# Kernel tuning notes

Measured on AMD Instinct MI355X. Metric: run time of the kernel, lower is better.

The kernel has to match this reference:

```python
import jax, jax.numpy as jnp
import numpy as np

B, S, D = 2, 2048, 1024
H = 16
HD = D // H  # 64
FORESIGHT = -1e9  # masked_fill value for non-causal positions


def setup_inputs() -> dict:
    key = jax.random.key(0)
    ks = jax.random.split(key, 8)
    s = 0.02
    return {
        "x": jax.random.normal(ks[0], (B, S, D), dtype=jnp.float32),
        "Wq": jax.random.normal(ks[1], (D, H * HD), dtype=jnp.float32) * s,
        "bq": jax.random.normal(ks[2], (H * HD,), dtype=jnp.float32) * s,
        "Wk": jax.random.normal(ks[3], (D, H * HD), dtype=jnp.float32) * s,
        "Wv": jax.random.normal(ks[4], (D, H * HD), dtype=jnp.float32) * s,
        "Wo": jax.random.normal(ks[5], (H * HD, D), dtype=jnp.float32) * s,
        "bo": jax.random.normal(ks[6], (D,), dtype=jnp.float32) * s,
    }


def reference(x, Wq, bq, Wk, Wv, Wo, bo):
    b, s, _ = x.shape
    # projections -> [B, H, S, HD]
    q = (x @ Wq + bq).reshape(b, s, H, HD).transpose(0, 2, 1, 3)
    k = (x @ Wk).reshape(b, s, H, HD).transpose(0, 2, 1, 3)
    v = (x @ Wv).reshape(b, s, H, HD).transpose(0, 2, 1, 3)
    # scores [B, H, S, S]
    scores = jnp.einsum("bhqd,bhkd->bhqk", q, k) / jnp.sqrt(jnp.float32(HD))
    # ALiBi bias: slope_h * j (key position), broadcast over queries
    slopes = 2.0 ** (-8.0 * jnp.arange(1, H + 1, dtype=jnp.float32) / H)
    positions = jnp.arange(s, dtype=jnp.float32)
    scores = scores - slopes[None, :, None, None] * positions[None, None, None, :]
    # causal mask: fill strictly-upper triangle with foresight
    causal = jnp.tril(jnp.ones((s, s), dtype=bool))
    scores = jnp.where(causal[None, None, :, :], scores, FORESIGHT)
    attn = jax.nn.softmax(scores, axis=-1)
    out = jnp.einsum("bhqk,bhkd->bhqd", attn, v)
    out = out.transpose(0, 2, 1, 3).reshape(b, s, H * HD)
    return out @ Wo + bo
```

## Files before the change

### kernel.cpp

```cpp
#include <hip/hip_runtime.h>
#include <stdint.h>

#define DDIM 1024
#define HH 16
#define HDIM 64
#define SS 2048

typedef short bf16x8 __attribute__((ext_vector_type(8)));
typedef float f32x4 __attribute__((ext_vector_type(4)));
typedef unsigned short u16;

__device__ __forceinline__ unsigned f2bf(float f) {
  unsigned u = __builtin_bit_cast(unsigned, f);
  u = u + 0x7FFFu + ((u >> 16) & 1u);
  return u >> 16;
}

__device__ __forceinline__ unsigned cvt_pk_bf16(float a, float b) {
  unsigned r;
  asm("v_cvt_pk_bf16_f32 %0, %1, %2" : "=v"(r) : "v"(a), "v"(b));
  return r;
}

__device__ __forceinline__ void gload16(const void* g, void* l) {
  __builtin_amdgcn_global_load_lds(
      (const __attribute__((address_space(1))) unsigned int*)g,
      (__attribute__((address_space(3))) unsigned int*)l, 16, 0, 0);
}

__global__ void k_convert_x(const float* __restrict__ x, u16* __restrict__ xb) {
  int i = (blockIdx.x * 256 + threadIdx.x) * 4;
  float4 v = *(const float4*)(x + i);
  ushort4 o;
  o.x = (u16)f2bf(v.x); o.y = (u16)f2bf(v.y); o.z = (u16)f2bf(v.z); o.w = (u16)f2bf(v.w);
  *(ushort4*)(xb + i) = o;
}

__global__ void k_transpose_w(const float* __restrict__ w0, const float* __restrict__ w1,
                              const float* __restrict__ w2, const float* __restrict__ w3,
                              u16* __restrict__ wt) {
  __shared__ float t[64][65];
  int z = blockIdx.z;
  const float* src = (z == 0) ? w0 : (z == 1) ? w1 : (z == 2) ? w2 : w3;
  u16* dst = wt + (size_t)z * DDIM * DDIM;
  int k0 = blockIdx.x * 64, n0 = blockIdx.y * 64;
  int tid = threadIdx.x;
  int c4 = tid & 15, rr = tid >> 4;
  for (int rep = 0; rep < 4; rep++) {
    int r = rr + rep * 16;
    float4 v = *(const float4*)(src + (size_t)(k0 + r) * DDIM + n0 + c4 * 4);
    t[r][c4 * 4 + 0] = v.x; t[r][c4 * 4 + 1] = v.y;
    t[r][c4 * 4 + 2] = v.z; t[r][c4 * 4 + 3] = v.w;
  }
  __syncthreads();
  for (int rep = 0; rep < 4; rep++) {
    int n = rr + rep * 16;
    ushort4 o;
    o.x = (u16)f2bf(t[c4 * 4 + 0][n]); o.y = (u16)f2bf(t[c4 * 4 + 1][n]);
    o.z = (u16)f2bf(t[c4 * 4 + 2][n]); o.w = (u16)f2bf(t[c4 * 4 + 3][n]);
    *(ushort4*)(dst + (size_t)(n0 + n) * DDIM + k0 + c4 * 4) = o;
  }
}

template <int MODE>
__global__ __launch_bounds__(256, 2) void k_gemm(const u16* __restrict__ A,
                                                 const u16* __restrict__ BT,
                                                 const float* __restrict__ bias,
                                                 void* __restrict__ O0,
                                                 void* __restrict__ O1,
                                                 void* __restrict__ O2) {
  __shared__ __align__(16) u16 lA[128 * 64];
  __shared__ __align__(16) u16 lB[128 * 64];
  const int tid = threadIdx.x;
  const int l = tid & 63, w = tid >> 6;
  const int wm = w >> 1, wn = w & 1;
  const int m0 = blockIdx.x * 128, n0 = blockIdx.y * 128;
  const int lr = l >> 4, lc = l & 15;

  const int srow = l >> 3;
  const int scol = ((l & 7) ^ srow) * 8;

  f32x4 acc[4][4];
  for (int mi = 0; mi < 4; mi++)
    for (int ni = 0; ni < 4; ni++)
      acc[mi][ni] = f32x4{0.f, 0.f, 0.f, 0.f};

  for (int kk = 0; kk < 16; kk++) {
    const int k0 = kk * 64;
    for (int i = 0; i < 4; i++) {
      int c = w * 4 + i;
      gload16(A + (size_t)(m0 + c * 8 + srow) * DDIM + k0 + scol, (char*)lA + c * 1024);
      gload16(BT + (size_t)(n0 + c * 8 + srow) * DDIM + k0 + scol, (char*)lB + c * 1024);
    }
    __syncthreads();
    for (int ks = 0; ks < 2; ks++) {
      bf16x8 af[4], bfr[4];
      for (int mi = 0; mi < 4; mi++) {
        int row = wm * 64 + mi * 16 + lc;
        int slot = (ks * 4 + lr) ^ (row & 7);
        af[mi] = *(const bf16x8*)((const char*)lA + row * 128 + slot * 16);
      }
      for (int ni = 0; ni < 4; ni++) {
        int row = wn * 64 + ni * 16 + lc;
        int slot = (ks * 4 + lr) ^ (row & 7);
        bfr[ni] = *(const bf16x8*)((const char*)lB + row * 128 + slot * 16);
      }
      for (int mi = 0; mi < 4; mi++)
        for (int ni = 0; ni < 4; ni++)
          acc[mi][ni] = __builtin_amdgcn_mfma_f32_16x16x32_bf16(af[mi], bfr[ni], acc[mi][ni], 0, 0, 0);
    }
    __syncthreads();
  }

  if (MODE == 0) {
    const int which = blockIdx.y >> 3;
    if (which == 0) {
      u16* C = (u16*)O0;
      const float c1 = 0.18033688011112043f;
      for (int mi = 0; mi < 4; mi++)
        for (int ni = 0; ni < 4; ni++) {
          int nl = (n0 + wn * 64 + ni * 16 + lc) & 1023;
          float badd = bias[nl];
          for (int r = 0; r < 4; r++) {
            int m = m0 + wm * 64 + mi * 16 + lr * 4 + r;
            C[(size_t)m * DDIM + nl] = (u16)f2bf((acc[mi][ni][r] + badd) * c1);
          }
        }
    } else if (which == 1) {
      u16* C = (u16*)O1;
      for (int mi = 0; mi < 4; mi++)
        for (int ni = 0; ni < 4; ni++) {
          int nl = (n0 + wn * 64 + ni * 16 + lc) & 1023;
          for (int r = 0; r < 4; r++) {
            int m = m0 + wm * 64 + mi * 16 + lr * 4 + r;
            C[(size_t)m * DDIM + nl] = (u16)f2bf(acc[mi][ni][r]);
          }
        }
    } else {
      u16* C = (u16*)O2;
      for (int mi = 0; mi < 4; mi++)
        for (int ni = 0; ni < 4; ni++) {
          int nl = (n0 + wn * 64 + ni * 16 + lc) & 1023;
          int h = nl >> 6, hd = nl & 63;
          int m = m0 + wm * 64 + mi * 16 + lr * 4;
          int b = m >> 11, s = m & 2047;
          unsigned d0 = f2bf(acc[mi][ni][0]) | (f2bf(acc[mi][ni][1]) << 16);
          unsigned d1 = f2bf(acc[mi][ni][2]) | (f2bf(acc[mi][ni][3]) << 16);
          u16* p = C + ((size_t)((b * HH + h) * HDIM + hd)) * SS + s;
          *(unsigned*)(p) = d0;
          *(unsigned*)(p + 2) = d1;
        }
    }
  } else {
    float* C = (float*)O0;
    for (int mi = 0; mi < 4; mi++)
      for (int ni = 0; ni < 4; ni++) {
        int n = n0 + wn * 64 + ni * 16 + lc;
        float badd = bias[n];
        for (int r = 0; r < 4; r++) {
          int m = m0 + wm * 64 + mi * 16 + lr * 4 + r;
          C[(size_t)m * DDIM + n] = acc[mi][ni][r] + badd;
        }
      }
  }
}

__device__ __forceinline__ void attn_tile(int kt, bool masked, int kfhi,
                                          const char* lKc, const char* lVc, char* lPw,
                                          const bf16x8 qf[2], f32x4 of[4],
                                          float& mrun, float& lrun_lane,
                                          float slope2, int lr, int lc, int q_glob) {
  f32x4 sf[4];
#pragma unroll
  for (int kf = 0; kf < 4; kf++) sf[kf] = f32x4{0.f, 0.f, 0.f, 0.f};
  __builtin_amdgcn_s_setprio(1);
#pragma unroll
  for (int ks = 0; ks < 2; ks++)
#pragma unroll
    for (int kf = 0; kf < 4; kf++) {
      if (kf >= kfhi) continue;
      int key = kf * 16 + lc;
      int slot = (ks * 4 + lr) ^ (lc & 7);
      bf16x8 a = *(const bf16x8*)(lKc + key * 128 + slot * 16);
      sf[kf] = __builtin_amdgcn_mfma_f32_16x16x32_bf16(a, qf[ks], sf[kf], 0, 0, 0);
    }
  __builtin_amdgcn_s_setprio(0);

  const float base = -slope2 * (float)(kt * 64 + lr * 4);
  float tmax = -3.0e38f;
#pragma unroll
  for (int kf = 0; kf < 4; kf++) {
    if (kf >= kfhi) continue;
#pragma unroll
    for (int r = 0; r < 4; r++) {
      float sv = sf[kf][r] + (base - slope2 * (float)(kf * 16 + r));
      if (masked) {
        int key = kt * 64 + kf * 16 + lr * 4 + r;
        if (key > q_glob) sv = -3.0e38f;
      }
      sf[kf][r] = sv;
      tmax = fmaxf(tmax, sv);
    }
  }

  if (__any(tmax > mrun)) {
    float tcol = fmaxf(tmax, __shfl_xor(tmax, 16));
    tcol = fmaxf(tcol, __shfl_xor(tcol, 32));
    if (tcol > mrun) {
      float corr = exp2f(mrun - tcol);
      lrun_lane *= corr;
#pragma unroll
      for (int mf = 0; mf < 4; mf++) {
        of[mf][0] *= corr; of[mf][1] *= corr; of[mf][2] *= corr; of[mf][3] *= corr;
      }
      mrun = tcol;
    }
  }

  const int kfUp = (kfhi + 1) & ~1;
  f32x4 ps = f32x4{0.f, 0.f, 0.f, 0.f};
#pragma unroll
  for (int kf = 0; kf < 4; kf++) {
    if (kf >= kfUp) continue;
    uint2 uu;
    if (kf < kfhi) {
      float p0 = exp2f(sf[kf][0] - mrun);
      float p1 = exp2f(sf[kf][1] - mrun);
      float p2 = exp2f(sf[kf][2] - mrun);
      float p3 = exp2f(sf[kf][3] - mrun);
      ps[0] += p0; ps[1] += p1; ps[2] += p2; ps[3] += p3;
      uu.x = cvt_pk_bf16(p0, p1);
      uu.y = cvt_pk_bf16(p2, p3);
    } else {
      uu.x = 0u; uu.y = 0u;
    }
    int slot = ((kf * 2 + (lr >> 1)) ^ (lc & 7));
    *(uint2*)(lPw + lc * 128 + slot * 16 + (lr & 1) * 8) = uu;
  }
  lrun_lane += (ps[0] + ps[1]) + (ps[2] + ps[3]);

  const int kshi = kfUp >> 1;
  __builtin_amdgcn_s_setprio(1);
#pragma unroll
  for (int ks = 0; ks < 2; ks++) {
    if (ks >= kshi) continue;
    int slotp = (ks * 4 + lr) ^ (lc & 7);
    bf16x8 pb = *(const bf16x8*)(lPw + lc * 128 + slotp * 16);
#pragma unroll
    for (int mf = 0; mf < 4; mf++) {
      int hd = mf * 16 + lc;
      int slotv = (ks * 4 + lr) ^ (lc & 7);
      bf16x8 va = *(const bf16x8*)(lVc + hd * 128 + slotv * 16);
      of[mf] = __builtin_amdgcn_mfma_f32_16x16x32_bf16(va, pb, of[mf], 0, 0, 0);
    }
  }
  __builtin_amdgcn_s_setprio(0);
}

__global__ __launch_bounds__(256, 4) void k_attn(const u16* __restrict__ Q,
                                                 const u16* __restrict__ Kg,
                                                 const u16* __restrict__ Vt,
                                                 u16* __restrict__ AO) {
  __shared__ __align__(16) u16 lK[2][64 * 64];
  __shared__ __align__(16) u16 lV[2][64 * 64];
  __shared__ __align__(16) u16 lP[4][16 * 64];

  const int tid = threadIdx.x;
  const int l = tid & 63, w = tid >> 6;
  const int lr = l >> 4, lc = l & 15;
  const int id = blockIdx.x;
  const int bh = id & 31;
  const int s5 = (id >> 5) & 1;
  const int gg = id >> 6;
  const int qt = s5 ? (31 - gg) : gg;
  const int b = bh >> 4, h = bh & 15;

  const float slope2 = exp2f(-0.5f * (float)(h + 1)) * 1.4426950408889634f;
  const int q_glob = qt * 64 + w * 16 + lc;

  bf16x8 qf[2];
#pragma unroll
  for (int ks = 0; ks < 2; ks++)
    qf[ks] = *(const bf16x8*)(Q + (size_t)(b * SS + q_glob) * DDIM + h * HDIM + ks * 32 + lr * 8);

  f32x4 of[4];
#pragma unroll
  for (int mf = 0; mf < 4; mf++) of[mf] = f32x4{0.f, 0.f, 0.f, 0.f};
  float mrun = -3.0e38f, lrun_lane = 0.f;

  const int srow = l >> 3;
  const int scol = ((l & 7) ^ srow) * 8;
  const int nkt = qt + 1;
  char* lPw = (char*)lP[w];

  auto stage = [&](int kt, int bb) {
#pragma unroll
    for (int i = 0; i < 2; i++) {
      int c = i * 4 + w;
      gload16(Kg + (size_t)(b * SS + kt * 64 + c * 8 + srow) * DDIM + h * HDIM + scol,
              (char*)lK[bb] + c * 1024);
      gload16(Vt + ((size_t)bh * HDIM + c * 8 + srow) * SS + kt * 64 + scol,
              (char*)lV[bb] + c * 1024);
    }
  };

  stage(0, 0);
  stage(nkt > 1 ? 1 : 0, 1);

  for (int t = 0; t < nkt; t++) {
    asm volatile("s_waitcnt vmcnt(4)" ::: "memory");
    __builtin_amdgcn_s_barrier();
    asm volatile("" ::: "memory");
    const bool last = (t == nkt - 1);
    attn_tile(t, last, last ? (w + 1) : 4,
              (const char*)lK[t & 1], (const char*)lV[t & 1], lPw,
              qf, of, mrun, lrun_lane, slope2, lr, lc, q_glob);
    __builtin_amdgcn_s_barrier();
    asm volatile("" ::: "memory");
    int kts = t + 2;
    if (kts > nkt - 1) kts = nkt - 1;
    stage(kts, t & 1);
  }

  float lrun = lrun_lane;
  lrun += __shfl_xor(lrun, 16);
  lrun += __shfl_xor(lrun, 32);
  float inv = 1.f / lrun;
  u16* obase = AO + (size_t)(b * SS + q_glob) * DDIM + h * HDIM;
#pragma unroll
  for (int mf = 0; mf < 4; mf++) {
    uint2 uu;
    uu.x = cvt_pk_bf16(of[mf][0] * inv, of[mf][1] * inv);
    uu.y = cvt_pk_bf16(of[mf][2] * inv, of[mf][3] * inv);
    *(uint2*)(obase + mf * 16 + lr * 4) = uu;
  }
}

extern "C" void kernel_launch(void* const* d_in, const int* in_sizes, int n_in,
                              void* d_out, int out_size, void* d_ws, size_t ws_size,
                              hipStream_t stream) {
  const float* x  = (const float*)d_in[0];
  const float* Wq = (const float*)d_in[1];
  const float* bq = (const float*)d_in[2];
  const float* Wk = (const float*)d_in[3];
  const float* Wv = (const float*)d_in[4];
  const float* Wo = (const float*)d_in[5];
  const float* bo = (const float*)d_in[6];
  float* out = (float*)d_out;

  u16* ws = (u16*)d_ws;
  const size_t MEG = 1024 * 1024;
  u16* xb = ws;
  u16* WT = ws + 4 * MEG;
  u16* Qb = ws + 8 * MEG;
  u16* Kb = ws + 12 * MEG;
  u16* Vt = ws + 16 * MEG;
  u16* AO = ws + 20 * MEG;

  k_convert_x<<<dim3(4096), dim3(256), 0, stream>>>(x, xb);
  k_transpose_w<<<dim3(16, 16, 4), dim3(256), 0, stream>>>(Wq, Wk, Wv, Wo, WT);
  k_gemm<0><<<dim3(32, 24), dim3(256), 0, stream>>>(xb, WT, bq, (void*)Qb, (void*)Kb, (void*)Vt);
  k_attn<<<dim3(1024), dim3(256), 0, stream>>>(Qb, Kb, Vt, AO);
  k_gemm<1><<<dim3(32, 8), dim3(256), 0, stream>>>(AO, WT + 3 * MEG, bo, (void*)out, nullptr, nullptr);
}
```

Measured before the change: 121.7 us.

## Pair complementary causal query tiles per block to share K/V staging

Each attention block now handles two query tiles, gg and 31-gg, for the same head. The K/V tiles staged into LDS are reused by both query streams, which balances causal work per block and halves K/V global loads. The grid is halved to 512 blocks and the occupancy hint drops from 4 to 3, in exchange for more registers (two sets of accumulators) and a larger P buffer. This gives fewer resident waves and fewer blocks to spread across CUs.

```diff
diff --git a/kernel.cpp b/kernel.cpp
--- a/kernel.cpp
+++ b/kernel.cpp
@@ -165,15 +165,14 @@
   }
 }
 
-__device__ __forceinline__ void attn_tile(int kt, bool masked, int kfhi,
-                                          const char* lKc, const char* lVc, char* lPw,
-                                          const bf16x8 qf[2], f32x4 of[4],
-                                          float& mrun, float& lrun_lane,
-                                          float slope2, int lr, int lc, int q_glob) {
+__device__ __forceinline__ void attn_stream(int kt, bool masked, int kfhi,
+                                            const char* lKc, const char* lVc, char* lPw,
+                                            const bf16x8 qf[2], f32x4 of[4],
+                                            float& mrun, float& lrun_lane,
+                                            float slope2, int lr, int lc, int q_glob) {
   f32x4 sf[4];
 #pragma unroll
   for (int kf = 0; kf < 4; kf++) sf[kf] = f32x4{0.f, 0.f, 0.f, 0.f};
-  __builtin_amdgcn_s_setprio(1);
 #pragma unroll
   for (int ks = 0; ks < 2; ks++)
 #pragma unroll
@@ -184,7 +183,6 @@
       bf16x8 a = *(const bf16x8*)(lKc + key * 128 + slot * 16);
       sf[kf] = __builtin_amdgcn_mfma_f32_16x16x32_bf16(a, qf[ks], sf[kf], 0, 0, 0);
     }
-  __builtin_amdgcn_s_setprio(0);
 
   const float base = -slope2 * (float)(kt * 64 + lr * 4);
   float tmax = -3.0e38f;
@@ -240,7 +238,6 @@
   lrun_lane += (ps[0] + ps[1]) + (ps[2] + ps[3]);
 
   const int kshi = kfUp >> 1;
-  __builtin_amdgcn_s_setprio(1);
 #pragma unroll
   for (int ks = 0; ks < 2; ks++) {
     if (ks >= kshi) continue;
@@ -254,44 +251,50 @@
       of[mf] = __builtin_amdgcn_mfma_f32_16x16x32_bf16(va, pb, of[mf], 0, 0, 0);
     }
   }
-  __builtin_amdgcn_s_setprio(0);
-}
-
-__global__ __launch_bounds__(256, 4) void k_attn(const u16* __restrict__ Q,
+}
+
+__global__ __launch_bounds__(256, 3) void k_attn(const u16* __restrict__ Q,
                                                  const u16* __restrict__ Kg,
                                                  const u16* __restrict__ Vt,
                                                  u16* __restrict__ AO) {
   __shared__ __align__(16) u16 lK[2][64 * 64];
   __shared__ __align__(16) u16 lV[2][64 * 64];
-  __shared__ __align__(16) u16 lP[4][16 * 64];
+  __shared__ __align__(16) u16 lP[4][2][16 * 64];
 
   const int tid = threadIdx.x;
   const int l = tid & 63, w = tid >> 6;
   const int lr = l >> 4, lc = l & 15;
   const int id = blockIdx.x;
   const int bh = id & 31;
-  const int s5 = (id >> 5) & 1;
-  const int gg = id >> 6;
-  const int qt = s5 ? (31 - gg) : gg;
+  const int gg = id >> 5;
+  const int qtA = gg, qtB = 31 - gg;
   const int b = bh >> 4, h = bh & 15;
 
   const float slope2 = exp2f(-0.5f * (float)(h + 1)) * 1.4426950408889634f;
-  const int q_glob = qt * 64 + w * 16 + lc;
-
-  bf16x8 qf[2];
-#pragma unroll
-  for (int ks = 0; ks < 2; ks++)
-    qf[ks] = *(const bf16x8*)(Q + (size_t)(b * SS + q_glob) * DDIM + h * HDIM + ks * 32 + lr * 8);
-
-  f32x4 of[4];
-#pragma unroll
-  for (int mf = 0; mf < 4; mf++) of[mf] = f32x4{0.f, 0.f, 0.f, 0.f};
-  float mrun = -3.0e38f, lrun_lane = 0.f;
+  const int q_globA = qtA * 64 + w * 16 + lc;
+  const int q_globB = qtB * 64 + w * 16 + lc;
+
+  bf16x8 qfA[2], qfB[2];
+#pragma unroll
+  for (int ks = 0; ks < 2; ks++) {
+    qfA[ks] = *(const bf16x8*)(Q + (size_t)(b * SS + q_globA) * DDIM + h * HDIM + ks * 32 + lr * 8);
+    qfB[ks] = *(const bf16x8*)(Q + (size_t)(b * SS + q_globB) * DDIM + h * HDIM + ks * 32 + lr * 8);
+  }
+
+  f32x4 ofA[4], ofB[4];
+#pragma unroll
+  for (int mf = 0; mf < 4; mf++) {
+    ofA[mf] = f32x4{0.f, 0.f, 0.f, 0.f};
+    ofB[mf] = f32x4{0.f, 0.f, 0.f, 0.f};
+  }
+  float mrunA = -3.0e38f, lrA = 0.f;
+  float mrunB = -3.0e38f, lrB = 0.f;
 
   const int srow = l >> 3;
   const int scol = ((l & 7) ^ srow) * 8;
-  const int nkt = qt + 1;
-  char* lPw = (char*)lP[w];
+  const int nkt = qtB + 1;
+  char* lPA = (char*)lP[w][0];
+  char* lPB = (char*)lP[w][1];
 
   auto stage = [&](int kt, int bb) {
 #pragma unroll
@@ -305,16 +308,26 @@
   };
 
   stage(0, 0);
-  stage(nkt > 1 ? 1 : 0, 1);
+  stage(1, 1);
 
   for (int t = 0; t < nkt; t++) {
     asm volatile("s_waitcnt vmcnt(4)" ::: "memory");
     __builtin_amdgcn_s_barrier();
     asm volatile("" ::: "memory");
-    const bool last = (t == nkt - 1);
-    attn_tile(t, last, last ? (w + 1) : 4,
-              (const char*)lK[t & 1], (const char*)lV[t & 1], lPw,
-              qf, of, mrun, lrun_lane, slope2, lr, lc, q_glob);
+    const char* Kc = (const char*)lK[t & 1];
+    const char* Vc = (const char*)lV[t & 1];
+    __builtin_amdgcn_s_setprio(1);
+    {
+      const bool lastB = (t == qtB);
+      attn_stream(t, lastB, lastB ? (w + 1) : 4, Kc, Vc, lPB,
+                  qfB, ofB, mrunB, lrB, slope2, lr, lc, q_globB);
+      if (t <= qtA) {
+        const bool lastA = (t == qtA);
+        attn_stream(t, lastA, lastA ? (w + 1) : 4, Kc, Vc, lPA,
+                    qfA, ofA, mrunA, lrA, slope2, lr, lc, q_globA);
+      }
+    }
+    __builtin_amdgcn_s_setprio(0);
     __builtin_amdgcn_s_barrier();
     asm volatile("" ::: "memory");
     int kts = t + 2;
@@ -322,17 +335,33 @@
     stage(kts, t & 1);
   }
 
-  float lrun = lrun_lane;
-  lrun += __shfl_xor(lrun, 16);
-  lrun += __shfl_xor(lrun, 32);
-  float inv = 1.f / lrun;
-  u16* obase = AO + (size_t)(b * SS + q_glob) * DDIM + h * HDIM;
-#pragma unroll
-  for (int mf = 0; mf < 4; mf++) {
-    uint2 uu;
-    uu.x = cvt_pk_bf16(of[mf][0] * inv, of[mf][1] * inv);
-    uu.y = cvt_pk_bf16(of[mf][2] * inv, of[mf][3] * inv);
-    *(uint2*)(obase + mf * 16 + lr * 4) = uu;
+  {
+    float lrun = lrA;
+    lrun += __shfl_xor(lrun, 16);
+    lrun += __shfl_xor(lrun, 32);
+    float inv = 1.f / lrun;
+    u16* obase = AO + (size_t)(b * SS + q_globA) * DDIM + h * HDIM;
+#pragma unroll
+    for (int mf = 0; mf < 4; mf++) {
+      uint2 uu;
+      uu.x = cvt_pk_bf16(ofA[mf][0] * inv, ofA[mf][1] * inv);
+      uu.y = cvt_pk_bf16(ofA[mf][2] * inv, ofA[mf][3] * inv);
+      *(uint2*)(obase + mf * 16 + lr * 4) = uu;
+    }
+  }
+  {
+    float lrun = lrB;
+    lrun += __shfl_xor(lrun, 16);
+    lrun += __shfl_xor(lrun, 32);
+    float inv = 1.f / lrun;
+    u16* obase = AO + (size_t)(b * SS + q_globB) * DDIM + h * HDIM;
+#pragma unroll
+    for (int mf = 0; mf < 4; mf++) {
+      uint2 uu;
+      uu.x = cvt_pk_bf16(ofB[mf][0] * inv, ofB[mf][1] * inv);
+      uu.y = cvt_pk_bf16(ofB[mf][2] * inv, ofB[mf][3] * inv);
+      *(uint2*)(obase + mf * 16 + lr * 4) = uu;
+    }
   }
 }
 
@@ -360,6 +389,6 @@
   k_convert_x<<<dim3(4096), dim3(256), 0, stream>>>(x, xb);
   k_transpose_w<<<dim3(16, 16, 4), dim3(256), 0, stream>>>(Wq, Wk, Wv, Wo, WT);
   k_gemm<0><<<dim3(32, 24), dim3(256), 0, stream>>>(xb, WT, bq, (void*)Qb, (void*)Kb, (void*)Vt);
-  k_attn<<<dim3(1024), dim3(256), 0, stream>>>(Qb, Kb, Vt, AO);
+  k_attn<<<dim3(512), dim3(256), 0, stream>>>(Qb, Kb, Vt, AO);
   k_gemm<1><<<dim3(32, 8), dim3(256), 0, stream>>>(AO, WT + 3 * MEG, bo, (void*)out, nullptr, nullptr);
 }
```

Result: slower. 126.0 us (+3.6%).

## Rewrite attention with 32x32 MFMA, register-resident P via permlane swap

Applied to the files above, without the earlier changes.

The attention kernel now gives each wave 32 queries and uses 32x32x16 bf16 MFMAs for both QK^T and PV. The P matrix is repacked in registers with v_permlane32_swap instead of a round trip through LDS. Each block now covers 128 queries and its four waves share one K/V stream, so the grid halves to 512 blocks and launch bounds drop to 2 blocks per CU. The goal is fewer LDS accesses and MFMA instructions per tile and more K/V reuse. The costs are more registers per wave, lower occupancy, and waves in a block sitting idle on different numbers of tiles.

```diff
diff --git a/kernel.cpp b/kernel.cpp
--- a/kernel.cpp
+++ b/kernel.cpp
@@ -8,6 +8,7 @@
 
 typedef short bf16x8 __attribute__((ext_vector_type(8)));
 typedef float f32x4 __attribute__((ext_vector_type(4)));
+typedef float f32x16 __attribute__((ext_vector_type(16)));
 typedef unsigned short u16;
 
 __device__ __forceinline__ unsigned f2bf(float f) {
@@ -22,10 +23,21 @@
   return r;
 }
 
+__device__ __forceinline__ void pswap(unsigned& a, unsigned& b) {
+  asm volatile("v_permlane32_swap_b32 %0, %1" : "+v"(a), "+v"(b));
+}
+
 __device__ __forceinline__ void gload16(const void* g, void* l) {
   __builtin_amdgcn_global_load_lds(
       (const __attribute__((address_space(1))) unsigned int*)g,
       (__attribute__((address_space(3))) unsigned int*)l, 16, 0, 0);
+}
+
+__device__ __forceinline__ f32x16 zero16() {
+  f32x16 z;
+#pragma unroll
+  for (int r = 0; r < 16; r++) z[r] = 0.f;
+  return z;
 }
 
 __global__ void k_convert_x(const float* __restrict__ x, u16* __restrict__ xb) {
@@ -165,133 +177,43 @@
   }
 }
 
-__device__ __forceinline__ void attn_tile(int kt, bool masked, int kfhi,
-                                          const char* lKc, const char* lVc, char* lPw,
-                                          const bf16x8 qf[2], f32x4 of[4],
-                                          float& mrun, float& lrun_lane,
-                                          float slope2, int lr, int lc, int q_glob) {
-  f32x4 sf[4];
-#pragma unroll
-  for (int kf = 0; kf < 4; kf++) sf[kf] = f32x4{0.f, 0.f, 0.f, 0.f};
-  __builtin_amdgcn_s_setprio(1);
-#pragma unroll
-  for (int ks = 0; ks < 2; ks++)
-#pragma unroll
-    for (int kf = 0; kf < 4; kf++) {
-      if (kf >= kfhi) continue;
-      int key = kf * 16 + lc;
-      int slot = (ks * 4 + lr) ^ (lc & 7);
-      bf16x8 a = *(const bf16x8*)(lKc + key * 128 + slot * 16);
-      sf[kf] = __builtin_amdgcn_mfma_f32_16x16x32_bf16(a, qf[ks], sf[kf], 0, 0, 0);
-    }
-  __builtin_amdgcn_s_setprio(0);
-
-  const float base = -slope2 * (float)(kt * 64 + lr * 4);
-  float tmax = -3.0e38f;
-#pragma unroll
-  for (int kf = 0; kf < 4; kf++) {
-    if (kf >= kfhi) continue;
-#pragma unroll
-    for (int r = 0; r < 4; r++) {
-      float sv = sf[kf][r] + (base - slope2 * (float)(kf * 16 + r));
-      if (masked) {
-        int key = kt * 64 + kf * 16 + lr * 4 + r;
-        if (key > q_glob) sv = -3.0e38f;
-      }
-      sf[kf][r] = sv;
-      tmax = fmaxf(tmax, sv);
-    }
-  }
-
-  if (__any(tmax > mrun)) {
-    float tcol = fmaxf(tmax, __shfl_xor(tmax, 16));
-    tcol = fmaxf(tcol, __shfl_xor(tcol, 32));
-    if (tcol > mrun) {
-      float corr = exp2f(mrun - tcol);
-      lrun_lane *= corr;
-#pragma unroll
-      for (int mf = 0; mf < 4; mf++) {
-        of[mf][0] *= corr; of[mf][1] *= corr; of[mf][2] *= corr; of[mf][3] *= corr;
-      }
-      mrun = tcol;
-    }
-  }
-
-  const int kfUp = (kfhi + 1) & ~1;
-  f32x4 ps = f32x4{0.f, 0.f, 0.f, 0.f};
-#pragma unroll
-  for (int kf = 0; kf < 4; kf++) {
-    if (kf >= kfUp) continue;
-    uint2 uu;
-    if (kf < kfhi) {
-      float p0 = exp2f(sf[kf][0] - mrun);
-      float p1 = exp2f(sf[kf][1] - mrun);
-      float p2 = exp2f(sf[kf][2] - mrun);
-      float p3 = exp2f(sf[kf][3] - mrun);
-      ps[0] += p0; ps[1] += p1; ps[2] += p2; ps[3] += p3;
-      uu.x = cvt_pk_bf16(p0, p1);
-      uu.y = cvt_pk_bf16(p2, p3);
-    } else {
-      uu.x = 0u; uu.y = 0u;
-    }
-    int slot = ((kf * 2 + (lr >> 1)) ^ (lc & 7));
-    *(uint2*)(lPw + lc * 128 + slot * 16 + (lr & 1) * 8) = uu;
-  }
-  lrun_lane += (ps[0] + ps[1]) + (ps[2] + ps[3]);
-
-  const int kshi = kfUp >> 1;
-  __builtin_amdgcn_s_setprio(1);
-#pragma unroll
-  for (int ks = 0; ks < 2; ks++) {
-    if (ks >= kshi) continue;
-    int slotp = (ks * 4 + lr) ^ (lc & 7);
-    bf16x8 pb = *(const bf16x8*)(lPw + lc * 128 + slotp * 16);
-#pragma unroll
-    for (int mf = 0; mf < 4; mf++) {
-      int hd = mf * 16 + lc;
-      int slotv = (ks * 4 + lr) ^ (lc & 7);
-      bf16x8 va = *(const bf16x8*)(lVc + hd * 128 + slotv * 16);
-      of[mf] = __builtin_amdgcn_mfma_f32_16x16x32_bf16(va, pb, of[mf], 0, 0, 0);
-    }
-  }
-  __builtin_amdgcn_s_setprio(0);
-}
-
-__global__ __launch_bounds__(256, 4) void k_attn(const u16* __restrict__ Q,
+__global__ __launch_bounds__(256, 2) void k_attn(const u16* __restrict__ Q,
                                                  const u16* __restrict__ Kg,
                                                  const u16* __restrict__ Vt,
                                                  u16* __restrict__ AO) {
   __shared__ __align__(16) u16 lK[2][64 * 64];
   __shared__ __align__(16) u16 lV[2][64 * 64];
-  __shared__ __align__(16) u16 lP[4][16 * 64];
 
   const int tid = threadIdx.x;
   const int l = tid & 63, w = tid >> 6;
-  const int lr = l >> 4, lc = l & 15;
+  const int lq = l & 31, hi = l >> 5;
   const int id = blockIdx.x;
   const int bh = id & 31;
-  const int s5 = (id >> 5) & 1;
-  const int gg = id >> 6;
-  const int qt = s5 ? (31 - gg) : gg;
+  const int gslot = id >> 5;
+  const int g = (gslot < 8) ? gslot : 23 - gslot;
   const int b = bh >> 4, h = bh & 15;
+  const int sw = g * 4 + w;
+  const int qglob = sw * 32 + lq;
+  const int nktw = (sw >> 1) + 1;
+  const int nkt = 2 * g + 2;
 
   const float slope2 = exp2f(-0.5f * (float)(h + 1)) * 1.4426950408889634f;
-  const int q_glob = qt * 64 + w * 16 + lc;
-
-  bf16x8 qf[2];
-#pragma unroll
-  for (int ks = 0; ks < 2; ks++)
-    qf[ks] = *(const bf16x8*)(Q + (size_t)(b * SS + q_glob) * DDIM + h * HDIM + ks * 32 + lr * 8);
-
-  f32x4 of[4];
-#pragma unroll
-  for (int mf = 0; mf < 4; mf++) of[mf] = f32x4{0.f, 0.f, 0.f, 0.f};
-  float mrun = -3.0e38f, lrun_lane = 0.f;
+  const float sh4 = slope2 * (float)(4 * hi);
+
+  f32x16 scr;
+#pragma unroll
+  for (int r = 0; r < 16; r++) scr[r] = slope2 * (float)((r & 3) + 8 * (r >> 2));
+
+  bf16x8 qf[4];
+#pragma unroll
+  for (int sd = 0; sd < 4; sd++)
+    qf[sd] = *(const bf16x8*)(Q + (size_t)(b * SS + qglob) * DDIM + h * HDIM + sd * 16 + hi * 8);
+
+  f32x16 o0 = zero16(), o1 = zero16();
+  float mrun = -3.0e38f, lrl = 0.f;
 
   const int srow = l >> 3;
   const int scol = ((l & 7) ^ srow) * 8;
-  const int nkt = qt + 1;
-  char* lPw = (char*)lP[w];
 
   auto stage = [&](int kt, int bb) {
 #pragma unroll
@@ -305,16 +227,123 @@
   };
 
   stage(0, 0);
-  stage(nkt > 1 ? 1 : 0, 1);
+  stage(1, 1);
 
   for (int t = 0; t < nkt; t++) {
     asm volatile("s_waitcnt vmcnt(4)" ::: "memory");
     __builtin_amdgcn_s_barrier();
     asm volatile("" ::: "memory");
-    const bool last = (t == nkt - 1);
-    attn_tile(t, last, last ? (w + 1) : 4,
-              (const char*)lK[t & 1], (const char*)lV[t & 1], lPw,
-              qf, of, mrun, lrun_lane, slope2, lr, lc, q_glob);
+    if (t < nktw) {
+      const char* Kc = (const char*)lK[t & 1];
+      const char* Vc = (const char*)lV[t & 1];
+      const bool lastp = (t == nktw - 1);
+      const bool doT1 = !lastp || (sw & 1);
+      const bool mT0 = lastp && !(sw & 1);
+      const bool mT1 = lastp && (sw & 1);
+
+      f32x16 s0 = zero16(), s1 = zero16();
+      __builtin_amdgcn_s_setprio(1);
+#pragma unroll
+      for (int sd = 0; sd < 4; sd++) {
+        int row = lq;
+        int slot = (2 * sd + hi) ^ (row & 7);
+        bf16x8 a = *(const bf16x8*)(Kc + row * 128 + slot * 16);
+        s0 = __builtin_amdgcn_mfma_f32_32x32x16_bf16(a, qf[sd], s0, 0, 0, 0);
+      }
+      if (doT1) {
+#pragma unroll
+        for (int sd = 0; sd < 4; sd++) {
+          int row = 32 + lq;
+          int slot = (2 * sd + hi) ^ (row & 7);
+          bf16x8 a = *(const bf16x8*)(Kc + row * 128 + slot * 16);
+          s1 = __builtin_amdgcn_mfma_f32_32x32x16_bf16(a, qf[sd], s1, 0, 0, 0);
+        }
+      }
+      __builtin_amdgcn_s_setprio(0);
+
+      const float bt0 = -slope2 * (float)(t * 64) - sh4;
+      const float bt1 = bt0 - slope2 * 32.f;
+      float tmax = -3.0e38f;
+#pragma unroll
+      for (int r = 0; r < 16; r++) {
+        float sv = (s0[r] + bt0) - scr[r];
+        if (mT0) {
+          int key = t * 64 + (r & 3) + 8 * (r >> 2) + 4 * hi;
+          if (key > qglob) sv = -3.0e38f;
+        }
+        s0[r] = sv;
+        tmax = fmaxf(tmax, sv);
+      }
+      if (doT1) {
+#pragma unroll
+        for (int r = 0; r < 16; r++) {
+          float sv = (s1[r] + bt1) - scr[r];
+          if (mT1) {
+            int key = t * 64 + 32 + (r & 3) + 8 * (r >> 2) + 4 * hi;
+            if (key > qglob) sv = -3.0e38f;
+          }
+          s1[r] = sv;
+          tmax = fmaxf(tmax, sv);
+        }
+      }
+      float tcol = fmaxf(tmax, __shfl_xor(tmax, 32));
+      if (__any(tcol > mrun)) {
+        float mnew = fmaxf(mrun, tcol);
+        float corr = exp2f(mrun - mnew);
+        lrl *= corr;
+#pragma unroll
+        for (int r = 0; r < 16; r++) { o0[r] *= corr; o1[r] *= corr; }
+        mrun = mnew;
+      }
+
+      f32x4 ps = f32x4{0.f, 0.f, 0.f, 0.f};
+#pragma unroll
+      for (int r = 0; r < 16; r++) {
+        float p = exp2f(s0[r] - mrun);
+        s0[r] = p;
+        ps[r & 3] += p;
+      }
+      if (doT1) {
+#pragma unroll
+        for (int r = 0; r < 16; r++) {
+          float p = exp2f(s1[r] - mrun);
+          s1[r] = p;
+          ps[r & 3] += p;
+        }
+      }
+      lrl += (ps[0] + ps[1]) + (ps[2] + ps[3]);
+
+      __builtin_amdgcn_s_setprio(1);
+      auto pvstep = [&](const f32x16& cs, int s) {
+        const int b8 = (s & 1) * 8;
+        unsigned x1 = cvt_pk_bf16(cs[b8 + 0], cs[b8 + 1]);
+        unsigned y1 = cvt_pk_bf16(cs[b8 + 4], cs[b8 + 5]);
+        pswap(x1, y1);
+        unsigned x2 = cvt_pk_bf16(cs[b8 + 2], cs[b8 + 3]);
+        unsigned y2 = cvt_pk_bf16(cs[b8 + 6], cs[b8 + 7]);
+        pswap(x2, y2);
+        uint4 pw; pw.x = x1; pw.y = x2; pw.z = y1; pw.w = y2;
+        bf16x8 pb = __builtin_bit_cast(bf16x8, pw);
+        int slotb = 2 * s + hi;
+        {
+          int row = lq;
+          bf16x8 va = *(const bf16x8*)(Vc + row * 128 + ((slotb ^ (row & 7)) << 4));
+          o0 = __builtin_amdgcn_mfma_f32_32x32x16_bf16(va, pb, o0, 0, 0, 0);
+        }
+        {
+          int row = 32 + lq;
+          bf16x8 va = *(const bf16x8*)(Vc + row * 128 + ((slotb ^ (row & 7)) << 4));
+          o1 = __builtin_amdgcn_mfma_f32_32x32x16_bf16(va, pb, o1, 0, 0, 0);
+        }
+      };
+      pvstep(s0, 0);
+      pvstep(s0, 1);
+      if (doT1) {
+        pvstep(s1, 2);
+        pvstep(s1, 3);
+      }
+      __builtin_amdgcn_s_setprio(0);
+    }
     __builtin_amdgcn_s_barrier();
     asm volatile("" ::: "memory");
     int kts = t + 2;
@@ -322,17 +351,18 @@
     stage(kts, t & 1);
   }
 
-  float lrun = lrun_lane;
-  lrun += __shfl_xor(lrun, 16);
-  lrun += __shfl_xor(lrun, 32);
-  float inv = 1.f / lrun;
-  u16* obase = AO + (size_t)(b * SS + q_glob) * DDIM + h * HDIM;
-#pragma unroll
-  for (int mf = 0; mf < 4; mf++) {
+  float lcol = lrl + __shfl_xor(lrl, 32);
+  float inv = 1.f / lcol;
+  u16* obase = AO + (size_t)(b * SS + qglob) * DDIM + h * HDIM;
+#pragma unroll
+  for (int rg = 0; rg < 4; rg++) {
     uint2 uu;
-    uu.x = cvt_pk_bf16(of[mf][0] * inv, of[mf][1] * inv);
-    uu.y = cvt_pk_bf16(of[mf][2] * inv, of[mf][3] * inv);
-    *(uint2*)(obase + mf * 16 + lr * 4) = uu;
+    uu.x = cvt_pk_bf16(o0[4 * rg + 0] * inv, o0[4 * rg + 1] * inv);
+    uu.y = cvt_pk_bf16(o0[4 * rg + 2] * inv, o0[4 * rg + 3] * inv);
+    *(uint2*)(obase + rg * 8 + 4 * hi) = uu;
+    uu.x = cvt_pk_bf16(o1[4 * rg + 0] * inv, o1[4 * rg + 1] * inv);
+    uu.y = cvt_pk_bf16(o1[4 * rg + 2] * inv, o1[4 * rg + 3] * inv);
+    *(uint2*)(obase + 32 + rg * 8 + 4 * hi) = uu;
   }
 }
 
@@ -360,6 +390,6 @@
   k_convert_x<<<dim3(4096), dim3(256), 0, stream>>>(x, xb);
   k_transpose_w<<<dim3(16, 16, 4), dim3(256), 0, stream>>>(Wq, Wk, Wv, Wo, WT);
   k_gemm<0><<<dim3(32, 24), dim3(256), 0, stream>>>(xb, WT, bq, (void*)Qb, (void*)Kb, (void*)Vt);
-  k_attn<<<dim3(1024), dim3(256), 0, stream>>>(Qb, Kb, Vt, AO);
+  k_attn<<<dim3(512), dim3(256), 0, stream>>>(Qb, Kb, Vt, AO);
   k_gemm<1><<<dim3(32, 8), dim3(256), 0, stream>>>(AO, WT + 3 * MEG, bo, (void*)out, nullptr, nullptr);
 }
```

Measured after the change: 133.6 us. 9.8% more time.

## Split causal attention KV range into chunks with separate combine kernel

Applied to the files above, without the earlier changes.

Attention work is split-KV style: each query tile's key range is divided into chunks of up to 8 key tiles, giving 2560 blocks instead of 1024. Each block writes an unnormalized fp32 partial output plus its running max and sum, and a new combine kernel merges the partials with log-sum-exp rescaling before writing bf16. The goal is better load balance and less of the long tail from the causal triangle, where late query tiles run much longer. In exchange it adds fp32 partial traffic through global memory, an extra kernel launch, and a serial scan loop in each attention block to decode its chunk index.

```diff
diff --git a/kernel.cpp b/kernel.cpp
--- a/kernel.cpp
+++ b/kernel.cpp
@@ -260,7 +260,8 @@
 __global__ __launch_bounds__(256, 4) void k_attn(const u16* __restrict__ Q,
                                                  const u16* __restrict__ Kg,
                                                  const u16* __restrict__ Vt,
-                                                 u16* __restrict__ AO) {
+                                                 float* __restrict__ Opart,
+                                                 float* __restrict__ Ml) {
   __shared__ __align__(16) u16 lK[2][64 * 64];
   __shared__ __align__(16) u16 lV[2][64 * 64];
   __shared__ __align__(16) u16 lP[4][16 * 64];
@@ -270,10 +271,13 @@
   const int lr = l >> 4, lc = l & 15;
   const int id = blockIdx.x;
   const int bh = id & 31;
-  const int s5 = (id >> 5) & 1;
-  const int gg = id >> 6;
-  const int qt = s5 ? (31 - gg) : gg;
+  int u = id >> 5;
+  int qt = 0, rem = u;
+  while (rem >= (qt >> 3) + 1) { rem -= (qt >> 3) + 1; qt++; }
+  const int c = rem;
   const int b = bh >> 4, h = bh & 15;
+  const int t0 = c * 8;
+  const int t1 = min(t0 + 8, qt + 1);
 
   const float slope2 = exp2f(-0.5f * (float)(h + 1)) * 1.4426950408889634f;
   const int q_glob = qt * 64 + w * 16 + lc;
@@ -290,50 +294,111 @@
 
   const int srow = l >> 3;
   const int scol = ((l & 7) ^ srow) * 8;
-  const int nkt = qt + 1;
   char* lPw = (char*)lP[w];
 
   auto stage = [&](int kt, int bb) {
 #pragma unroll
     for (int i = 0; i < 2; i++) {
-      int c = i * 4 + w;
-      gload16(Kg + (size_t)(b * SS + kt * 64 + c * 8 + srow) * DDIM + h * HDIM + scol,
-              (char*)lK[bb] + c * 1024);
-      gload16(Vt + ((size_t)bh * HDIM + c * 8 + srow) * SS + kt * 64 + scol,
-              (char*)lV[bb] + c * 1024);
+      int cc = i * 4 + w;
+      gload16(Kg + (size_t)(b * SS + kt * 64 + cc * 8 + srow) * DDIM + h * HDIM + scol,
+              (char*)lK[bb] + cc * 1024);
+      gload16(Vt + ((size_t)bh * HDIM + cc * 8 + srow) * SS + kt * 64 + scol,
+              (char*)lV[bb] + cc * 1024);
     }
   };
 
-  stage(0, 0);
-  stage(nkt > 1 ? 1 : 0, 1);
-
-  for (int t = 0; t < nkt; t++) {
+  stage(t0, 0);
+  stage(t0 + 1 < t1 ? t0 + 1 : t0, 1);
+
+  for (int t = t0; t < t1; t++) {
     asm volatile("s_waitcnt vmcnt(4)" ::: "memory");
     __builtin_amdgcn_s_barrier();
     asm volatile("" ::: "memory");
-    const bool last = (t == nkt - 1);
+    const bool last = (t == qt);
     attn_tile(t, last, last ? (w + 1) : 4,
               (const char*)lK[t & 1], (const char*)lV[t & 1], lPw,
               qf, of, mrun, lrun_lane, slope2, lr, lc, q_glob);
     __builtin_amdgcn_s_barrier();
     asm volatile("" ::: "memory");
     int kts = t + 2;
-    if (kts > nkt - 1) kts = nkt - 1;
+    if (kts > t1 - 1) kts = t1 - 1;
     stage(kts, t & 1);
   }
 
   float lrun = lrun_lane;
   lrun += __shfl_xor(lrun, 16);
   lrun += __shfl_xor(lrun, 32);
-  float inv = 1.f / lrun;
-  u16* obase = AO + (size_t)(b * SS + q_glob) * DDIM + h * HDIM;
+  float* Op = Opart + (size_t)id * 4096 + (w * 16 + lc) * 64;
 #pragma unroll
   for (int mf = 0; mf < 4; mf++) {
-    uint2 uu;
-    uu.x = cvt_pk_bf16(of[mf][0] * inv, of[mf][1] * inv);
-    uu.y = cvt_pk_bf16(of[mf][2] * inv, of[mf][3] * inv);
-    *(uint2*)(obase + mf * 16 + lr * 4) = uu;
-  }
+    float4 v;
+    v.x = of[mf][0]; v.y = of[mf][1]; v.z = of[mf][2]; v.w = of[mf][3];
+    *(float4*)(Op + mf * 16 + lr * 4) = v;
+  }
+  if (lr == 0) {
+    float2 mlv; mlv.x = mrun; mlv.y = lrun;
+    *(float2*)(Ml + (size_t)id * 128 + (w * 16 + lc) * 2) = mlv;
+  }
+}
+
+__global__ __launch_bounds__(256, 4) void k_combine(const float* __restrict__ Opart,
+                                                    const float* __restrict__ Ml,
+                                                    u16* __restrict__ AO) {
+  const int blk = blockIdx.x;
+  const int bh = blk & 31, qt = blk >> 5;
+  const int b = bh >> 4, h = bh & 15;
+  const int a = qt >> 3;
+  const int nc = a + 1;
+  const int base = (a + 1) * (4 * a + (qt & 7));
+  const int tid = threadIdx.x;
+  const int q = tid >> 2, seg = (tid & 3) << 4;
+
+  float m0 = -3.0e38f, m1 = -3.0e38f, m2 = -3.0e38f, m3 = -3.0e38f;
+  float l0 = 0.f, l1 = 0.f, l2 = 0.f, l3 = 0.f;
+#pragma unroll 4
+  for (int cc = 0; cc < 4; cc++) {
+    if (cc >= nc) continue;
+    int sid = (base + cc) * 32 + bh;
+    float2 mlv = *(const float2*)(Ml + (size_t)sid * 128 + q * 2);
+    if (cc == 0) { m0 = mlv.x; l0 = mlv.y; }
+    else if (cc == 1) { m1 = mlv.x; l1 = mlv.y; }
+    else if (cc == 2) { m2 = mlv.x; l2 = mlv.y; }
+    else { m3 = mlv.x; l3 = mlv.y; }
+  }
+  float mstar = fmaxf(fmaxf(m0, m1), fmaxf(m2, m3));
+  float s0 = exp2f(m0 - mstar), s1 = exp2f(m1 - mstar);
+  float s2 = exp2f(m2 - mstar), s3 = exp2f(m3 - mstar);
+
+  float acc[16];
+#pragma unroll
+  for (int r = 0; r < 16; r++) acc[r] = 0.f;
+  float lstar = 0.f;
+#pragma unroll 4
+  for (int cc = 0; cc < 4; cc++) {
+    if (cc >= nc) continue;
+    float sc = (cc == 0) ? s0 : (cc == 1) ? s1 : (cc == 2) ? s2 : s3;
+    lstar += ((cc == 0) ? l0 : (cc == 1) ? l1 : (cc == 2) ? l2 : l3) * sc;
+    int sid = (base + cc) * 32 + bh;
+    const float* Op = Opart + (size_t)sid * 4096 + q * 64 + seg;
+#pragma unroll
+    for (int r4 = 0; r4 < 4; r4++) {
+      float4 v = *(const float4*)(Op + r4 * 4);
+      acc[r4 * 4 + 0] += v.x * sc;
+      acc[r4 * 4 + 1] += v.y * sc;
+      acc[r4 * 4 + 2] += v.z * sc;
+      acc[r4 * 4 + 3] += v.w * sc;
+    }
+  }
+  float inv = 1.f / lstar;
+  unsigned pk[8];
+#pragma unroll
+  for (int i = 0; i < 8; i++)
+    pk[i] = f2bf(acc[2 * i] * inv) | (f2bf(acc[2 * i + 1] * inv) << 16);
+  u16* ab = AO + (size_t)(b * SS + qt * 64 + q) * DDIM + h * HDIM + seg;
+  uint4 w0; w0.x = pk[0]; w0.y = pk[1]; w0.z = pk[2]; w0.w = pk[3];
+  uint4 w1; w1.x = pk[4]; w1.y = pk[5]; w1.z = pk[6]; w1.w = pk[7];
+  *(uint4*)(ab) = w0;
+  *(uint4*)(ab + 8) = w1;
 }
 
 extern "C" void kernel_launch(void* const* d_in, const int* in_sizes, int n_in,
@@ -356,10 +421,13 @@
   u16* Kb = ws + 12 * MEG;
   u16* Vt = ws + 16 * MEG;
   u16* AO = ws + 20 * MEG;
+  float* Opart = (float*)(ws + 24 * MEG);
+  float* Ml    = Opart + (size_t)2560 * 4096;
 
   k_convert_x<<<dim3(4096), dim3(256), 0, stream>>>(x, xb);
   k_transpose_w<<<dim3(16, 16, 4), dim3(256), 0, stream>>>(Wq, Wk, Wv, Wo, WT);
   k_gemm<0><<<dim3(32, 24), dim3(256), 0, stream>>>(xb, WT, bq, (void*)Qb, (void*)Kb, (void*)Vt);
-  k_attn<<<dim3(1024), dim3(256), 0, stream>>>(Qb, Kb, Vt, AO);
+  k_attn<<<dim3(2560), dim3(256), 0, stream>>>(Qb, Kb, Vt, Opart, Ml);
+  k_combine<<<dim3(1024), dim3(256), 0, stream>>>(Opart, Ml, AO);
   k_gemm<1><<<dim3(32, 8), dim3(256), 0, stream>>>(AO, WT + 3 * MEG, bo, (void*)out, nullptr, nullptr);
 }
```

Result: slower. 129.6 us (+6.5%).
